# Performance work log

Hardware: AMD Instinct MI355X
Metric: run time of the kernel (lower is better)

## Reference

```python
import jax, jax.numpy as jnp
import numpy as np

B, S, D_IN, D_OUT, H = 4, 2048, 1024, 1024, 16
HD = D_OUT // H


def setup_inputs() -> dict:
    key = jax.random.key(0)
    ks = jax.random.split(key, 6)
    s = 1.0 / np.sqrt(D_IN)
    x = jax.random.normal(ks[0], (B, S, D_IN), dtype=jnp.float32)
    Wq = jax.random.uniform(ks[1], (D_OUT, D_IN), jnp.float32, -s, s)  # torch Linear weight [out,in]
    Wk = jax.random.uniform(ks[2], (D_OUT, D_IN), jnp.float32, -s, s)
    Wv = jax.random.uniform(ks[3], (D_OUT, D_IN), jnp.float32, -s, s)
    so = 1.0 / np.sqrt(D_OUT)
    Wo = jax.random.uniform(ks[4], (D_OUT, D_OUT), jnp.float32, -so, so)
    bo = jax.random.uniform(ks[5], (D_OUT,), jnp.float32, -so, so)
    return {"x": x, "Wq": Wq, "Wk": Wk, "Wv": Wv, "Wo": Wo, "bo": bo}


def reference(x, Wq, Wk, Wv, Wo, bo):
    b, n, _ = x.shape
    # projections (torch Linear: x @ W^T), split heads -> [b, h, n, hd]
    def heads(y):
        return y.reshape(b, n, H, HD).transpose(0, 2, 1, 3)
    q = heads(x @ Wq.T)
    k = heads(x @ Wk.T)
    v = heads(x @ Wv.T)
    scores = jnp.einsum('bhqd,bhkd->bhqk', q, k)
    causal = jnp.triu(jnp.ones((n, n), dtype=bool), k=1)
    scores = jnp.where(causal, -jnp.inf, scores)
    attn = jax.nn.softmax(scores / np.sqrt(HD), axis=-1)  # dropout p=0.0 -> identity
    ctx = jnp.einsum('bhqk,bhkd->bhqd', attn, v)
    ctx = ctx.transpose(0, 2, 1, 3).reshape(b, n, D_OUT)
    return ctx @ Wo.T + bo
```

## Files before the change

kernel.cpp:

```cpp
#include <hip/hip_runtime.h>
#include <hip/hip_bf16.h>
#include <stdint.h>

#define B_N 4
#define SEQ 2048
#define DMODEL 1024
#define NHEAD 16
#define HDIM 64
#define BHEADS (B_N * NHEAD)
#define MROWS (B_N * SEQ)

typedef short bf16x8_t __attribute__((ext_vector_type(8)));
typedef float f32x4_t __attribute__((ext_vector_type(4)));

static __device__ __forceinline__ unsigned short f2bf(float f) {
  __hip_bfloat16 h = __float2bfloat16(f);
  return __builtin_bit_cast(unsigned short, h);
}

#define GLDS16(gp, lp)                                                        \
  __builtin_amdgcn_global_load_lds(                                           \
      (const __attribute__((address_space(1))) unsigned int*)(gp),            \
      (__attribute__((address_space(3))) unsigned int*)(lp), 16, 0, 0)

__global__ void cast_f32_bf16_v4(const float* __restrict__ in,
                                 unsigned short* __restrict__ out, int n4,
                                 float scale) {
  int i = blockIdx.x * blockDim.x + threadIdx.x;
  if (i >= n4) return;
  float4 v = reinterpret_cast<const float4*>(in)[i];
  ushort4 o;
  o.x = f2bf(v.x * scale); o.y = f2bf(v.y * scale);
  o.z = f2bf(v.z * scale); o.w = f2bf(v.w * scale);
  reinterpret_cast<ushort4*>(out)[i] = o;
}

__global__ void cast_weights(const float* __restrict__ Wq,
                             const float* __restrict__ Wk,
                             const float* __restrict__ Wv,
                             const float* __restrict__ Wo,
                             unsigned short* __restrict__ out) {
  int i = blockIdx.x * blockDim.x + threadIdx.x;
  int mat = i >> 18;
  int off = i & 262143;
  const float* src = (mat == 0) ? Wq : (mat == 1) ? Wk : (mat == 2) ? Wv : Wo;
  float scale = (mat == 0) ? 0.125f : 1.0f;
  float4 v = reinterpret_cast<const float4*>(src)[off];
  ushort4 o;
  o.x = f2bf(v.x * scale); o.y = f2bf(v.y * scale);
  o.z = f2bf(v.z * scale); o.w = f2bf(v.w * scale);
  reinterpret_cast<ushort4*>(out)[i] = o;
}


#define SLOT_B 24576
#define NSLOTS 6

#define PH_READ(AFL, BFL)                                                     \
  {                                                                           \
    const char* cb = smem_c + rs * SLOT_B;                                    \
    _Pragma("unroll")                                                         \
    for (int rt = 0; rt < 4; rt++)                                            \
      AFL[rt] = *(const bf16x8_t*)(cb + offA[rt]);                            \
    _Pragma("unroll")                                                         \
    for (int ct = 0; ct < 4; ct++)                                            \
      BFL[ct] = *(const bf16x8_t*)(cb + offB[ct]);                            \
    if (++rs == NSLOTS) rs = 0;                                               \
  }

#define PH_GLDS(hh)                                                           \
  {                                                                           \
    char* sb = smem_c + gs * SLOT_B;                                          \
    GLDS16(aB + (size_t)(hh) * 32, sb + t * 16);                              \
    GLDS16(b0B + (size_t)(hh) * 32, sb + 8192 + t * 16);                      \
    GLDS16(b1B + (size_t)(hh) * 32, sb + 16384 + t * 16);                     \
    if (++gs == NSLOTS) gs = 0;                                               \
  }

#define PH_MFMA(AFU, BFU)                                                     \
  __builtin_amdgcn_sched_barrier(0);                                          \
  __builtin_amdgcn_s_setprio(1);                                              \
  _Pragma("unroll")                                                           \
  for (int rt = 0; rt < 4; rt++)                                              \
    _Pragma("unroll")                                                         \
    for (int ct = 0; ct < 4; ct++)                                            \
      acc[rt][ct] = __builtin_amdgcn_mfma_f32_16x16x32_bf16(                  \
          AFU[rt], BFU[ct], acc[rt][ct], 0, 0, 0);                            \
  __builtin_amdgcn_s_setprio(0);

#define CERT(N)                                                               \
  asm volatile("s_waitcnt vmcnt(" #N ")" ::: "memory");                       \
  __builtin_amdgcn_s_barrier();                                               \
  asm volatile("" ::: "memory");

#define GEMM_PIPE_BODY                                                        \
  _Pragma("unroll")                                                           \
  for (int h = 0; h < 4; ++h) {                                               \
    char* sb = smem_c + h * SLOT_B;                                           \
    GLDS16(aB + (size_t)h * 32, sb + t * 16);                                 \
    GLDS16(b0B + (size_t)h * 32, sb + 8192 + t * 16);                         \
    GLDS16(b1B + (size_t)h * 32, sb + 16384 + t * 16);                        \
  }                                                                           \
  int rs = 0, gs = 4;                                                         \
  bf16x8_t afX[4], bfX[4], afY[4], bfY[4];                                    \
  CERT(9)                                                                     \
  PH_READ(afX, bfX)                                                           \
  for (int i = 0; i < 14; ++i) {                                              \
    CERT(6) PH_READ(afY, bfY) PH_GLDS(2 * i + 4) PH_MFMA(afX, bfX)            \
    CERT(6) PH_READ(afX, bfX) PH_GLDS(2 * i + 5) PH_MFMA(afY, bfY)            \
  }                                                                           \
  CERT(6) PH_READ(afY, bfY) PH_MFMA(afX, bfX)                   \
  CERT(3) PH_READ(afX, bfX) PH_MFMA(afY, bfY)                   \
  CERT(0) PH_READ(afY, bfY) PH_MFMA(afX, bfX)                   \
  PH_MFMA(afY, bfY)

__global__ __launch_bounds__(512, 2)
void gemm_qkv(const unsigned short* __restrict__ A,
              const unsigned short* __restrict__ W,
              unsigned short* __restrict__ Out) {
  __shared__ __align__(16) unsigned short smem[73728];
  char* smem_c = (char*)smem;

  const int t = threadIdx.x;
  const int lane = t & 63;
  const int w = t >> 6;
  const int quad = lane >> 4;
  const int l16 = lane & 15;
  const int rowBase = blockIdx.x * 128;
  const int colBase = blockIdx.y * 256;
  const int wr = (w >> 2) * 64;
  const int wc = (w & 3) * 64;
  const int K = DMODEL;

  const int srow = t >> 2;
  const int ssw = ((t & 3) ^ ((t >> 3) & 3)) * 8;
  const unsigned short* aB  = A + (size_t)(rowBase + srow) * K + ssw;
  const unsigned short* b0B = W + (size_t)(colBase + srow) * K + ssw;
  const unsigned short* b1B = W + (size_t)(colBase + 128 + srow) * K + ssw;

  const int swz = (quad ^ ((l16 >> 1) & 3)) * 16;
  int offA[4], offB[4];
#pragma unroll
  for (int rt = 0; rt < 4; rt++) offA[rt] = (wr + rt * 16 + l16) * 64 + swz;
#pragma unroll
  for (int ct = 0; ct < 4; ct++)
    offB[ct] = 8192 + (wc + ct * 16 + l16) * 64 + swz;

  f32x4_t zero4 = {0.f, 0.f, 0.f, 0.f};
  f32x4_t acc[4][4];
#pragma unroll
  for (int i = 0; i < 4; i++)
#pragma unroll
    for (int j = 0; j < 4; j++) acc[i][j] = zero4;

  GEMM_PIPE_BODY

  __syncthreads();

  const int mat = colBase >> 10;
  const int nl = colBase & 1023;
  const int hh = (nl + wc) >> 6;
  const int bb = rowBase >> 11;

  if (mat == 2) {
    unsigned short* T = smem + w * 4608;
#pragma unroll
    for (int ct = 0; ct < 4; ct++)
#pragma unroll
      for (int rt = 0; rt < 4; rt++) {
        ushort4 pk;
        pk.x = f2bf(acc[rt][ct][0]);
        pk.y = f2bf(acc[rt][ct][1]);
        pk.z = f2bf(acc[rt][ct][2]);
        pk.w = f2bf(acc[rt][ct][3]);
        *(ushort4*)&T[(ct * 16 + l16) * 72 + rt * 16 + quad * 4] = pk;
      }
    const int srw = (rowBase & (SEQ - 1)) + wr;
    unsigned short* Cq = Out + 2 * (size_t)MROWS * DMODEL;
#pragma unroll
    for (int it = 0; it < 8; it++) {
      int nn = it * 8 + (lane >> 3);
      int sg = lane & 7;
      uint4 d = *(const uint4*)&T[nn * 72 + sg * 8];
      *(uint4*)(Cq + ((size_t)(bb * NHEAD + hh) * HDIM + nn) * SEQ + srw +
                sg * 8) = d;
    }
  } else {
    unsigned short* T = smem + w * 4608;
#pragma unroll
    for (int rt = 0; rt < 4; rt++)
#pragma unroll
      for (int ct = 0; ct < 4; ct++)
#pragma unroll
        for (int r = 0; r < 4; r++)
          T[(rt * 16 + quad * 4 + r) * 72 + ct * 16 + l16] =
              f2bf(acc[rt][ct][r]);
    unsigned short* Cq = Out + (size_t)mat * MROWS * DMODEL;
#pragma unroll
    for (int it = 0; it < 8; it++) {
      int idx = it * 64 + lane;
      int row = idx >> 3, sg = idx & 7, sgx = sg ^ (row & 7);
      uint4 d = *(const uint4*)&T[row * 72 + sgx * 8];
      int m = rowBase + wr + row;
      int s = m & (SEQ - 1), b = m >> 11;
      *(uint4*)(Cq + (((size_t)(b * NHEAD + hh)) * SEQ + s) * HDIM + sgx * 8) = d;
    }
  }
}

__global__ __launch_bounds__(512, 2)
void gemm_out(const unsigned short* __restrict__ A,
              const unsigned short* __restrict__ Bw,
              float* __restrict__ Cf, const float* __restrict__ bias) {
  __shared__ __align__(16) unsigned short smem[73728];
  char* smem_c = (char*)smem;

  const int t = threadIdx.x;
  const int lane = t & 63;
  const int w = t >> 6;
  const int quad = lane >> 4;
  const int l16 = lane & 15;
  const int rowBase = blockIdx.x * 128;
  const int colBase = blockIdx.y * 256;
  const int wr = (w >> 2) * 64;
  const int wc = (w & 3) * 64;
  const int K = DMODEL, N = DMODEL;

  const int srow = t >> 2;
  const int ssw = ((t & 3) ^ ((t >> 3) & 3)) * 8;
  const unsigned short* aB  = A + (size_t)(rowBase + srow) * K + ssw;
  const unsigned short* b0B = Bw + (size_t)(colBase + srow) * K + ssw;
  const unsigned short* b1B = Bw + (size_t)(colBase + 128 + srow) * K + ssw;

  const int swz = (quad ^ ((l16 >> 1) & 3)) * 16;
  int offA[4], offB[4];
#pragma unroll
  for (int rt = 0; rt < 4; rt++) offA[rt] = (wr + rt * 16 + l16) * 64 + swz;
#pragma unroll
  for (int ct = 0; ct < 4; ct++)
    offB[ct] = 8192 + (wc + ct * 16 + l16) * 64 + swz;

  f32x4_t zero4 = {0.f, 0.f, 0.f, 0.f};
  f32x4_t acc[4][4];
#pragma unroll
  for (int i = 0; i < 4; i++)
#pragma unroll
    for (int j = 0; j < 4; j++) acc[i][j] = zero4;

  GEMM_PIPE_BODY

#pragma unroll
  for (int rt = 0; rt < 4; rt++)
#pragma unroll
    for (int ct = 0; ct < 4; ct++) {
      int n = colBase + wc + ct * 16 + l16;
      float bv = bias[n];
#pragma unroll
      for (int r = 0; r < 4; r++) {
        int m = rowBase + wr + rt * 16 + quad * 4 + r;
        Cf[(size_t)m * N + n] = acc[rt][ct][r] + bv;
      }
    }
}

__global__ __launch_bounds__(256, 3)
void attn_kernel(const unsigned short* __restrict__ Qg_,
                 const unsigned short* __restrict__ Kg_,
                 const unsigned short* __restrict__ Vtg_,
                 unsigned short* __restrict__ ctx) {
  __shared__ __align__(16) unsigned short Ks[2][4096];
  __shared__ __align__(16) unsigned short Vs[2][4096];
  __shared__ __align__(16) unsigned short Ps[4][2048];

  const int t = threadIdx.x;
  const int lane = t & 63, w = t >> 6;
  const int quad = lane >> 4, l16 = lane & 15;
  const int sw = l16 & 7;
  unsigned short* PsW = &Ps[w][0];

  const int rank = blockIdx.x;
  const int qt = 15 - (rank >> 6);
  const int bh = rank & 63;
  const int nt = 2 * qt + 2;
  const size_t base = (size_t)bh * SEQ * HDIM;

  const int r0 = t >> 3;
  const int s0 = ((t & 7) ^ (r0 & 7)) * 8;
  const int r1 = r0 + 32;

  const unsigned short* Kg = Kg_ + base;
  const unsigned short* Vg = Vtg_ + base;

  GLDS16(Kg + r0 * HDIM + s0, (char*)&Ks[0][0] + t * 16);
  GLDS16(Kg + r1 * HDIM + s0, (char*)&Ks[0][0] + t * 16 + 4096);
  GLDS16(Vg + (size_t)r0 * SEQ + s0, (char*)&Vs[0][0] + t * 16);
  GLDS16(Vg + (size_t)r1 * SEQ + s0, (char*)&Vs[0][0] + t * 16 + 4096);

  const int q0w = qt * 128 + w * 32;

  bf16x8_t qf[2][2];
#pragma unroll
  for (int q2 = 0; q2 < 2; q2++)
#pragma unroll
    for (int kh = 0; kh < 2; kh++)
      qf[q2][kh] = *(const bf16x8_t*)(Qg_ + base +
          (size_t)(q0w + q2 * 16 + l16) * HDIM + kh * 32 + quad * 8);

  float l_[2] = {0.f, 0.f};
  f32x4_t zero4 = {0.f, 0.f, 0.f, 0.f};
  f32x4_t o[2][4];
#pragma unroll
  for (int q2 = 0; q2 < 2; q2++)
#pragma unroll
    for (int dt = 0; dt < 4; dt++) o[q2][dt] = zero4;

  int buf = 0;
  for (int jt = 0; jt < nt; ++jt) {
    __syncthreads();
    if (jt + 1 < nt) {
      const unsigned short* Kg2 = Kg + (size_t)(jt + 1) * 64 * HDIM;
      const unsigned short* Vg2 = Vg + (jt + 1) * 64;
      char* kd = (char*)&Ks[buf ^ 1][0] + t * 16;
      char* vd = (char*)&Vs[buf ^ 1][0] + t * 16;
      GLDS16(Kg2 + r0 * HDIM + s0, kd);
      GLDS16(Kg2 + r1 * HDIM + s0, kd + 4096);
      GLDS16(Vg2 + (size_t)r0 * SEQ + s0, vd);
      GLDS16(Vg2 + (size_t)r1 * SEQ + s0, vd + 4096);
    }

    if (jt * 64 <= q0w + 31) {
      const unsigned short* Kb = &Ks[buf][0];
      const unsigned short* Vb = &Vs[buf][0];
      f32x4_t sc[2][4];
#pragma unroll
      for (int q2 = 0; q2 < 2; q2++)
#pragma unroll
        for (int kt = 0; kt < 4; kt++) sc[q2][kt] = zero4;

#pragma unroll
      for (int kt = 0; kt < 4; kt++)
#pragma unroll
        for (int kh = 0; kh < 2; kh++) {
          bf16x8_t kf = *(const bf16x8_t*)((const char*)Kb +
              ((kt * 16 + l16) * 64 + (((kh * 4 + quad) ^ sw) * 8)) * 2);
          sc[0][kt] = __builtin_amdgcn_mfma_f32_16x16x32_bf16(
              kf, qf[0][kh], sc[0][kt], 0, 0, 0);
          sc[1][kt] = __builtin_amdgcn_mfma_f32_16x16x32_bf16(
              kf, qf[1][kh], sc[1][kt], 0, 0, 0);
        }

      if (jt * 64 + 63 > q0w) {
#pragma unroll
        for (int q2 = 0; q2 < 2; q2++) {
          int q = q0w + q2 * 16 + l16;
#pragma unroll
          for (int kt = 0; kt < 4; kt++)
#pragma unroll
            for (int r = 0; r < 4; r++) {
              int key = jt * 64 + kt * 16 + quad * 4 + r;
              if (key > q) sc[q2][kt][r] = -3.0e38f;
            }
        }
      }

#pragma unroll
      for (int q2 = 0; q2 < 2; q2++) {
        float sum = 0.f;
#pragma unroll
        for (int kt = 0; kt < 4; kt++) {
          float p0 = __expf(sc[q2][kt][0]);
          float p1 = __expf(sc[q2][kt][1]);
          float p2 = __expf(sc[q2][kt][2]);
          float p3 = __expf(sc[q2][kt][3]);
          sum += p0 + p1 + p2 + p3;
          ushort4 pk;
          pk.x = f2bf(p0); pk.y = f2bf(p1); pk.z = f2bf(p2); pk.w = f2bf(p3);
          int u = (kt * 4 + quad) ^ ((l16 & 7) << 1);
          *(ushort4*)&PsW[q2 * 1024 + l16 * 64 + u * 4] = pk;
        }
        sum += __shfl_xor(sum, 16, 64);
        sum += __shfl_xor(sum, 32, 64);
        l_[q2] += sum;
      }

      bf16x8_t pf[2][2];
#pragma unroll
      for (int q2 = 0; q2 < 2; q2++)
#pragma unroll
        for (int kc = 0; kc < 2; kc++) {
          int u = (kc * 8 + quad * 2) ^ ((l16 & 7) << 1);
          pf[q2][kc] = *(const bf16x8_t*)&PsW[q2 * 1024 + l16 * 64 + u * 4];
        }
#pragma unroll
      for (int dt = 0; dt < 4; dt++)
#pragma unroll
        for (int kc = 0; kc < 2; kc++) {
          bf16x8_t vfrag = *(const bf16x8_t*)((const char*)Vb +
              ((dt * 16 + l16) * 64 + (((kc * 4 + quad) ^ sw) * 8)) * 2);
          o[0][dt] = __builtin_amdgcn_mfma_f32_16x16x32_bf16(
              vfrag, pf[0][kc], o[0][dt], 0, 0, 0);
          o[1][dt] = __builtin_amdgcn_mfma_f32_16x16x32_bf16(
              vfrag, pf[1][kc], o[1][dt], 0, 0, 0);
        }
    }
    buf ^= 1;
  }

  const int bidx = bh >> 4, h = bh & 15;
#pragma unroll
  for (int q2 = 0; q2 < 2; q2++) {
    float inv = 1.0f / l_[q2];
#pragma unroll
    for (int dt = 0; dt < 4; dt++) {
      ushort4 pk;
      pk.x = f2bf(o[q2][dt][0] * inv);
      pk.y = f2bf(o[q2][dt][1] * inv);
      pk.z = f2bf(o[q2][dt][2] * inv);
      pk.w = f2bf(o[q2][dt][3] * inv);
      int u = (dt * 4 + quad) ^ ((l16 & 7) << 1);
      *(ushort4*)&PsW[q2 * 1024 + l16 * 64 + u * 4] = pk;
    }
  }
  {
    int qq = lane >> 2, sg = lane & 3;
#pragma unroll
    for (int q2 = 0; q2 < 2; q2++) {
      int ua = (sg * 2) ^ ((qq & 7) << 1);
      int ub = (sg * 2 + 8) ^ ((qq & 7) << 1);
      uint4 da = *(const uint4*)&PsW[q2 * 1024 + qq * 64 + ua * 4];
      uint4 db = *(const uint4*)&PsW[q2 * 1024 + qq * 64 + ub * 4];
      size_t rowoff =
          ((size_t)(bidx * SEQ + q0w + q2 * 16 + qq)) * DMODEL + h * HDIM;
      *(uint4*)(ctx + rowoff + sg * 8) = da;
      *(uint4*)(ctx + rowoff + (sg + 4) * 8) = db;
    }
  }
}

extern "C" void kernel_launch(void* const* d_in, const int* in_sizes, int n_in,
                              void* d_out, int out_size, void* d_ws,
                              size_t ws_size, hipStream_t stream) {
  const float* x  = (const float*)d_in[0];
  const float* Wq = (const float*)d_in[1];
  const float* Wk = (const float*)d_in[2];
  const float* Wv = (const float*)d_in[3];
  const float* Wo = (const float*)d_in[4];
  const float* bo = (const float*)d_in[5];
  float* out = (float*)d_out;

  const size_t XE = (size_t)MROWS * DMODEL;
  const size_t WE = (size_t)DMODEL * DMODEL;

  unsigned short* xb   = (unsigned short*)d_ws;
  unsigned short* wqb  = xb + XE;
  unsigned short* wob  = wqb + 3 * WE;
  unsigned short* Qb   = wqb + 4 * WE;
  unsigned short* Kb   = Qb + XE;
  unsigned short* Vtb  = Kb + XE;
  unsigned short* ctxb = xb;

  cast_f32_bf16_v4<<<(int)(XE / 4 + 255) / 256, 256, 0, stream>>>(x, xb,
      (int)(XE / 4), 1.0f);
  cast_weights<<<(int)(4 * WE / 4 + 255) / 256, 256, 0, stream>>>(Wq, Wk, Wv,
      Wo, wqb);

  gemm_qkv<<<dim3(MROWS / 128, 3 * DMODEL / 256), 512, 0, stream>>>(xb, wqb, Qb);

  attn_kernel<<<dim3(1024), 256, 0, stream>>>(Qb, Kb, Vtb, ctxb);

  gemm_out<<<dim3(MROWS / 128, DMODEL / 256), 512, 0, stream>>>(ctxb, wob, out, bo);
}
```

Before: 231.2 us.

## Shrink GEMM LDS pipeline to 3 slots and raise occupancy to 4 blocks

The GEMM main loop now uses a simpler 3-slot LDS ring with prefetch distance 2 in place of the 6-slot, double-register-buffered pipeline. LDS per block drops from 144KB to 72KB, and launch bounds go from 2 to 4 blocks per CU, so more blocks can run at once and hide latency across waves. In exchange, each iteration loses the overlap between its LDS reads and the MFMAs and adds a barrier. The tighter register budget at 4 blocks per CU may also cause spills.

After: 221.8 us. 1.04x faster.

```diff
diff --git a/kernel.cpp b/kernel.cpp
--- a/kernel.cpp
+++ b/kernel.cpp
@@ -54,39 +54,7 @@
 
 
 #define SLOT_B 24576
-#define NSLOTS 6
-
-#define PH_READ(AFL, BFL)                                                     \
-  {                                                                           \
-    const char* cb = smem_c + rs * SLOT_B;                                    \
-    _Pragma("unroll")                                                         \
-    for (int rt = 0; rt < 4; rt++)                                            \
-      AFL[rt] = *(const bf16x8_t*)(cb + offA[rt]);                            \
-    _Pragma("unroll")                                                         \
-    for (int ct = 0; ct < 4; ct++)                                            \
-      BFL[ct] = *(const bf16x8_t*)(cb + offB[ct]);                            \
-    if (++rs == NSLOTS) rs = 0;                                               \
-  }
-
-#define PH_GLDS(hh)                                                           \
-  {                                                                           \
-    char* sb = smem_c + gs * SLOT_B;                                          \
-    GLDS16(aB + (size_t)(hh) * 32, sb + t * 16);                              \
-    GLDS16(b0B + (size_t)(hh) * 32, sb + 8192 + t * 16);                      \
-    GLDS16(b1B + (size_t)(hh) * 32, sb + 16384 + t * 16);                     \
-    if (++gs == NSLOTS) gs = 0;                                               \
-  }
-
-#define PH_MFMA(AFU, BFU)                                                     \
-  __builtin_amdgcn_sched_barrier(0);                                          \
-  __builtin_amdgcn_s_setprio(1);                                              \
-  _Pragma("unroll")                                                           \
-  for (int rt = 0; rt < 4; rt++)                                              \
-    _Pragma("unroll")                                                         \
-    for (int ct = 0; ct < 4; ct++)                                            \
-      acc[rt][ct] = __builtin_amdgcn_mfma_f32_16x16x32_bf16(                  \
-          AFU[rt], BFU[ct], acc[rt][ct], 0, 0, 0);                            \
-  __builtin_amdgcn_s_setprio(0);
+#define NSLOTS 3
 
 #define CERT(N)                                                               \
   asm volatile("s_waitcnt vmcnt(" #N ")" ::: "memory");                       \
@@ -95,30 +63,55 @@
 
 #define GEMM_PIPE_BODY                                                        \
   _Pragma("unroll")                                                           \
-  for (int h = 0; h < 4; ++h) {                                               \
+  for (int h = 0; h < 2; ++h) {                                               \
     char* sb = smem_c + h * SLOT_B;                                           \
     GLDS16(aB + (size_t)h * 32, sb + t * 16);                                 \
     GLDS16(b0B + (size_t)h * 32, sb + 8192 + t * 16);                         \
     GLDS16(b1B + (size_t)h * 32, sb + 16384 + t * 16);                        \
   }                                                                           \
-  int rs = 0, gs = 4;                                                         \
-  bf16x8_t afX[4], bfX[4], afY[4], bfY[4];                                    \
-  CERT(9)                                                                     \
-  PH_READ(afX, bfX)                                                           \
-  for (int i = 0; i < 14; ++i) {                                              \
-    CERT(6) PH_READ(afY, bfY) PH_GLDS(2 * i + 4) PH_MFMA(afX, bfX)            \
-    CERT(6) PH_READ(afX, bfX) PH_GLDS(2 * i + 5) PH_MFMA(afY, bfY)            \
-  }                                                                           \
-  CERT(6) PH_READ(afY, bfY) PH_MFMA(afX, bfX)                   \
-  CERT(3) PH_READ(afX, bfX) PH_MFMA(afY, bfY)                   \
-  CERT(0) PH_READ(afY, bfY) PH_MFMA(afX, bfX)                   \
-  PH_MFMA(afY, bfY)
-
-__global__ __launch_bounds__(512, 2)
+  CERT(3)                                                                     \
+  {                                                                           \
+    int cur = 0, gs = 2;                                                      \
+    const int NH = 32;                                                        \
+    for (int h = 0; h < NH; ++h) {                                            \
+      const char* cb = smem_c + cur * SLOT_B;                                 \
+      bf16x8_t af[4], bfr[4];                                                 \
+      _Pragma("unroll")                                                       \
+      for (int rt = 0; rt < 4; rt++)                                          \
+        af[rt] = *(const bf16x8_t*)(cb + offA[rt]);                           \
+      _Pragma("unroll")                                                       \
+      for (int ct = 0; ct < 4; ct++)                                          \
+        bfr[ct] = *(const bf16x8_t*)(cb + offB[ct]);                          \
+      if (h + 2 < NH) {                                                       \
+        char* sb = smem_c + gs * SLOT_B;                                      \
+        GLDS16(aB + (size_t)(h + 2) * 32, sb + t * 16);                       \
+        GLDS16(b0B + (size_t)(h + 2) * 32, sb + 8192 + t * 16);               \
+        GLDS16(b1B + (size_t)(h + 2) * 32, sb + 16384 + t * 16);              \
+      }                                                                       \
+      __builtin_amdgcn_s_barrier();                                           \
+      asm volatile("s_waitcnt lgkmcnt(0)" ::: "memory");                      \
+      __builtin_amdgcn_sched_barrier(0);                                      \
+      __builtin_amdgcn_s_setprio(1);                                          \
+      _Pragma("unroll")                                                       \
+      for (int rt = 0; rt < 4; rt++)                                          \
+        _Pragma("unroll")                                                     \
+        for (int ct = 0; ct < 4; ct++)                                        \
+          acc[rt][ct] = __builtin_amdgcn_mfma_f32_16x16x32_bf16(              \
+              af[rt], bfr[ct], acc[rt][ct], 0, 0, 0);                         \
+      __builtin_amdgcn_s_setprio(0);                                          \
+      if (h + 1 < NH) {                                                       \
+        if (h + 2 < NH) { CERT(3) } else { CERT(0) }                          \
+      }                                                                       \
+      if (++cur == NSLOTS) cur = 0;                                           \
+      if (++gs == NSLOTS) gs = 0;                                             \
+    }                                                                         \
+  }
+
+__global__ __launch_bounds__(512, 4)
 void gemm_qkv(const unsigned short* __restrict__ A,
               const unsigned short* __restrict__ W,
               unsigned short* __restrict__ Out) {
-  __shared__ __align__(16) unsigned short smem[73728];
+  __shared__ __align__(16) unsigned short smem[36864];
   char* smem_c = (char*)smem;
 
   const int t = threadIdx.x;
@@ -208,11 +201,11 @@
   }
 }
 
-__global__ __launch_bounds__(512, 2)
+__global__ __launch_bounds__(512, 4)
 void gemm_out(const unsigned short* __restrict__ A,
               const unsigned short* __restrict__ Bw,
               float* __restrict__ Cf, const float* __restrict__ bias) {
-  __shared__ __align__(16) unsigned short smem[73728];
+  __shared__ __align__(16) unsigned short smem[36864];
   char* smem_c = (char*)smem;
 
   const int t = threadIdx.x;
```
